# Performance work log

Measured on AMD Instinct MI355X. Metric: run time of the kernel, lower is better.

Reference implementation:

```python
import jax, jax.numpy as jnp
import numpy as np

H, W, DIM, B, K = 28, 28, 384, 64, 1
EPS = 1e-5


def setup_inputs() -> dict:
    key = jax.random.key(0)
    k1, k2, k3 = jax.random.split(key, 3)
    L = 1 + K * H * W
    x = jax.random.normal(k1, (B, L, DIM), dtype=jnp.float32)
    w_reduction = jax.random.normal(k2, (2 * DIM, 4 * DIM), dtype=jnp.float32) * 0.02
    w_convert = jax.random.normal(k3, (2 * DIM, DIM), dtype=jnp.float32) * 0.02
    ln_gamma = jnp.ones((4 * DIM,), dtype=jnp.float32)
    ln_beta = jnp.zeros((4 * DIM,), dtype=jnp.float32)
    return {"x": x, "w_reduction": w_reduction, "w_convert": w_convert,
            "ln_gamma": ln_gamma, "ln_beta": ln_beta}


def reference(x, w_reduction, w_convert, ln_gamma, ln_beta):
    Bb, L, C = x.shape
    k = (L - 1) // (H * W)
    cls_token = x[:, 0:1, :]                      # [B,1,C]
    feat = x[:, 1:, :].reshape(Bb, k, H, W, C)
    x0 = feat[:, :, 0::2, 0::2, :]                # [B,k,H/2,W/2,C]
    x1 = feat[:, :, 1::2, 0::2, :]
    x2 = feat[:, :, 0::2, 1::2, :]
    x3 = feat[:, :, 1::2, 1::2, :]
    m = jnp.concatenate([x0, x1, x2, x3], axis=-1)  # [B,k,H/2,W/2,4C]
    m = m.reshape(Bb, k, -1, 4 * C)
    # LayerNorm over last dim
    mu = jnp.mean(m, axis=-1, keepdims=True)
    var = jnp.mean(jnp.square(m - mu), axis=-1, keepdims=True)
    m = (m - mu) * jax.lax.rsqrt(var + EPS) * ln_gamma + ln_beta
    red = jnp.einsum('bknf,of->bkno', m, w_reduction).reshape(Bb, -1, 2 * C)
    cls_out = jnp.einsum('bic,oc->bio', cls_token, w_convert)  # [B,1,2C]
    return jnp.concatenate([cls_out, red], axis=1)
```

## Files before the change

### kernel.cpp

```cpp
#include <hip/hip_runtime.h>
#include <hip/hip_bf16.h>

#define DIMC 384
#define LL 785
#define FDIM 1536
#define ODIM 768
#define NPATCH 196
#define MROWS 12544
#define BATCH 64

typedef __attribute__((ext_vector_type(8))) short bf16x8;
typedef __attribute__((ext_vector_type(4))) float floatx4;
typedef __attribute__((ext_vector_type(4))) unsigned short ushort4v;

#define WS_WBF_OFF  38535168
#define WS_BIAS_OFF 40894464

__device__ __forceinline__ unsigned short f2bf(float f) {
  union { float f; unsigned int u; } v; v.f = f;
  unsigned int u = v.u + 0x7fffu + ((v.u >> 16) & 1u);
  return (unsigned short)(u >> 16);
}

__device__ __forceinline__ void gload_lds16(const void* g, void* l) {
  __builtin_amdgcn_global_load_lds(
      (const __attribute__((address_space(1))) unsigned int*)g,
      (__attribute__((address_space(3))) unsigned int*)l, 16, 0, 0);
}

__global__ __launch_bounds__(256) void prep_kernel(
    const float* __restrict__ x, const float* __restrict__ wred,
    const float* __restrict__ wconv, const float* __restrict__ gamma,
    const float* __restrict__ beta, unsigned short* __restrict__ anorm,
    unsigned short* __restrict__ wbf, float* __restrict__ bias,
    float* __restrict__ out) {
  const int blk = blockIdx.x;
  const int t = threadIdx.x;
  const int wv = t >> 6;
  const int lane = t & 63;

  if (blk < 3136) {
    int gw = blk * 4 + wv;
    int b = gw / NPATCH;
    int n = gw - b * NPATCH;
    int i = n / 14;
    int j = n - i * 14;
    const float* xb = x + ((size_t)b * LL + 1) * DIMC;
    float4 v[6];
    float s = 0.f, s2 = 0.f;
#pragma unroll
    for (int c = 0; c < 6; ++c) {
      int f = lane * 4 + c * 256;
      int q = f / 384;
      int cc = f - q * 384;
      int off = ((i * 2 + (q & 1)) * 28 + (j * 2 + ((q >> 1) & 1))) * DIMC + cc;
      v[c] = *reinterpret_cast<const float4*>(xb + off);
      s  += v[c].x + v[c].y + v[c].z + v[c].w;
      s2 += v[c].x * v[c].x + v[c].y * v[c].y + v[c].z * v[c].z + v[c].w * v[c].w;
    }
#pragma unroll
    for (int o = 1; o < 64; o <<= 1) {
      s  += __shfl_xor(s, o);
      s2 += __shfl_xor(s2, o);
    }
    float mu = s * (1.f / FDIM);
    float var = s2 * (1.f / FDIM) - mu * mu;
    float rs = rsqrtf(var + 1e-5f);
    float nmu = -mu * rs;
    unsigned short* arow = anorm + (size_t)gw * FDIM;
#pragma unroll
    for (int c = 0; c < 6; ++c) {
      int f = lane * 4 + c * 256;
      union { ushort4v u4; __hip_bfloat162 h[2]; } u;
      u.h[0] = __float22bfloat162_rn(
          make_float2(v[c].x * rs + nmu, v[c].y * rs + nmu));
      u.h[1] = __float22bfloat162_rn(
          make_float2(v[c].z * rs + nmu, v[c].w * rs + nmu));
      *reinterpret_cast<ushort4v*>(arow + f) = u.u4;
    }
  } else if (blk < 4288) {
    int idx4 = (blk - 3136) * 256 + t;
    int e0 = idx4 * 4;
    int f = e0 % FDIM;
    float4 w = *reinterpret_cast<const float4*>(wred + e0);
    float4 g = *reinterpret_cast<const float4*>(gamma + f);
    ushort4v u;
    u.x = f2bf(w.x * g.x); u.y = f2bf(w.y * g.y);
    u.z = f2bf(w.z * g.z); u.w = f2bf(w.w * g.w);
    *reinterpret_cast<ushort4v*>(wbf + e0) = u;
  } else if (blk < 4480) {
    int o = (blk - 4288) * 4 + wv;
    const float* wr = wred + (size_t)o * FDIM;
    float s = 0.f;
#pragma unroll
    for (int c = 0; c < 6; ++c) {
      int f = lane * 4 + c * 256;
      float4 w = *reinterpret_cast<const float4*>(wr + f);
      float4 be = *reinterpret_cast<const float4*>(beta + f);
      s += w.x * be.x + w.y * be.y + w.z * be.z + w.w * be.w;
    }
#pragma unroll
    for (int o2 = 32; o2 > 0; o2 >>= 1) s += __shfl_down(s, o2);
    if (lane == 0) bias[o] = s;
  } else {
    __shared__ float xs[DIMC];
    int idx = blk - 4480;
    int b = idx / 3;
    int ch = idx - b * 3;
    for (int c = t; c < DIMC; c += 256) xs[c] = x[(size_t)b * LL * DIMC + c];
    __syncthreads();
    int o = ch * 256 + t;
    const float* wr = wconv + (size_t)o * DIMC;
    float acc = 0.f;
#pragma unroll 4
    for (int c = 0; c < DIMC; c += 4) {
      float4 w = *reinterpret_cast<const float4*>(wr + c);
      acc += w.x * xs[c] + w.y * xs[c + 1] + w.z * xs[c + 2] + w.w * xs[c + 3];
    }
    out[(size_t)b * 197 * ODIM + o] = acc;
  }
}

__global__ __launch_bounds__(256) void gemm_kernel(
    const unsigned short* __restrict__ anorm,
    const unsigned short* __restrict__ wbf,
    const float* __restrict__ bias, float* __restrict__ out) {
  __shared__ unsigned short As[128 * 64];
  __shared__ unsigned short Bs[128 * 64];

  const int t = threadIdx.x;
  const int mBase = blockIdx.y * 128;
  const int nBase = blockIdx.x * 128;

  const unsigned short* agp[4];
  const unsigned short* bgp[4];
  unsigned int ldsoff[4];
#pragma unroll
  for (int p = 0; p < 4; ++p) {
    int s = p * 256 + t;
    int r = s >> 3;
    int cs = (s & 7) ^ (r & 7);
    agp[p] = anorm + (size_t)(mBase + r) * FDIM + cs * 8;
    bgp[p] = wbf + (size_t)(nBase + r) * FDIM + cs * 8;
    ldsoff[p] = (unsigned)s * 8;
  }

  const int wv = t >> 6;
  const int lane = t & 63;
  const int ln15 = lane & 15;
  const int quad = lane >> 4;
  const int wm = wv >> 1;
  const int wn = wv & 1;

  unsigned int aoff[4][2], boff[4][2];
#pragma unroll
  for (int mt = 0; mt < 4; ++mt) {
#pragma unroll
    for (int h = 0; h < 2; ++h) {
      int rA = wm * 64 + mt * 16 + ln15;
      aoff[mt][h] = (unsigned)(rA * 64 + (((h * 4 + quad) ^ (rA & 7)) * 8));
      int rB = wn * 64 + mt * 16 + ln15;
      boff[mt][h] = (unsigned)(rB * 64 + (((h * 4 + quad) ^ (rB & 7)) * 8));
    }
  }

  floatx4 acc[4][4];
#pragma unroll
  for (int mt = 0; mt < 4; ++mt)
#pragma unroll
    for (int nt = 0; nt < 4; ++nt)
      acc[mt][nt] = floatx4{0.f, 0.f, 0.f, 0.f};

  for (int kt = 0; kt < FDIM / 64; ++kt) {
    if (kt) __syncthreads();
#pragma unroll
    for (int p = 0; p < 4; ++p) {
      gload_lds16(agp[p], &As[ldsoff[p]]);
      gload_lds16(bgp[p], &Bs[ldsoff[p]]);
      agp[p] += 64;
      bgp[p] += 64;
    }
    __syncthreads();

#pragma unroll
    for (int h = 0; h < 2; ++h) {
      bf16x8 af[4], bfr[4];
#pragma unroll
      for (int mt = 0; mt < 4; ++mt)
        af[mt] = *reinterpret_cast<const bf16x8*>(&As[aoff[mt][h]]);
#pragma unroll
      for (int nt = 0; nt < 4; ++nt)
        bfr[nt] = *reinterpret_cast<const bf16x8*>(&Bs[boff[nt][h]]);
#pragma unroll
      for (int mt = 0; mt < 4; ++mt)
#pragma unroll
        for (int nt = 0; nt < 4; ++nt)
          acc[mt][nt] = __builtin_amdgcn_mfma_f32_16x16x32_bf16(
              af[mt], bfr[nt], acc[mt][nt], 0, 0, 0);
    }
  }

  float bs[4];
#pragma unroll
  for (int nt = 0; nt < 4; ++nt)
    bs[nt] = bias[nBase + wn * 64 + nt * 16 + ln15];
#pragma unroll
  for (int mt = 0; mt < 4; ++mt) {
#pragma unroll
    for (int r = 0; r < 4; ++r) {
      int m = mBase + wm * 64 + mt * 16 + quad * 4 + r;
      int b = m / NPATCH;
      int n = m - b * NPATCH;
      float* orow = out + ((size_t)b * 197 + 1 + n) * ODIM + nBase + wn * 64;
#pragma unroll
      for (int nt = 0; nt < 4; ++nt)
        orow[nt * 16 + ln15] = acc[mt][nt][r] + bs[nt];
    }
  }
}

extern "C" void kernel_launch(void* const* d_in, const int* in_sizes, int n_in,
                              void* d_out, int out_size, void* d_ws, size_t ws_size,
                              hipStream_t stream) {
  const float* x     = (const float*)d_in[0];
  const float* wred  = (const float*)d_in[1];
  const float* wconv = (const float*)d_in[2];
  const float* gamma = (const float*)d_in[3];
  const float* beta  = (const float*)d_in[4];
  float* out = (float*)d_out;

  unsigned short* anorm = (unsigned short*)d_ws;
  unsigned short* wbf   = (unsigned short*)((char*)d_ws + WS_WBF_OFF);
  float* bias           = (float*)((char*)d_ws + WS_BIAS_OFF);

  prep_kernel<<<dim3(4672), 256, 0, stream>>>(x, wred, wconv, gamma, beta,
                                              anorm, wbf, bias, out);
  gemm_kernel<<<dim3(ODIM / 128, MROWS / 128), 256, 0, stream>>>(anorm, wbf,
                                                                 bias, out);
}
```

Before: 205.4 us.

## Rework prep blocks for multi-row norm and remap GEMM tiles per XCD

The prep kernel now has each wave process four LayerNorm rows, taking statistics in a first pass and then re-reading x for the normalize/store pass instead of holding values in registers. Block ranges are reordered so the cls GEMV and bias blocks come first, and the cls GEMV is vectorized with two accumulators. The GEMM uses a 1D grid with an XCD-aware tile remap so neighbouring tiles share the same L2, and stores the output with nontemporal stores. These changes target prep occupancy and launch count, L2 locality for the GEMM, and cache pollution from output writes, at the cost of a second read of x that relies on cache hits.

New measurement: 185.1 us. 9.9% less time.

```diff
diff --git a/kernel.cpp b/kernel.cpp
--- a/kernel.cpp
+++ b/kernel.cpp
@@ -15,6 +15,12 @@
 
 #define WS_WBF_OFF  38535168
 #define WS_BIAS_OFF 40894464
+
+#define PB_CLS   0
+#define PB_NORM  192
+#define PB_BIAS  976
+#define PB_WBF   1168
+#define PREP_BLOCKS 2320
 
 __device__ __forceinline__ unsigned short f2bf(float f) {
   union { float f; unsigned int u; } v; v.f = f;
@@ -39,47 +45,102 @@
   const int wv = t >> 6;
   const int lane = t & 63;
 
-  if (blk < 3136) {
-    int gw = blk * 4 + wv;
-    int b = gw / NPATCH;
-    int n = gw - b * NPATCH;
-    int i = n / 14;
-    int j = n - i * 14;
-    const float* xb = x + ((size_t)b * LL + 1) * DIMC;
-    float4 v[6];
-    float s = 0.f, s2 = 0.f;
+  if (blk >= PB_NORM && blk < PB_BIAS) {
+    int radd[6];
 #pragma unroll
     for (int c = 0; c < 6; ++c) {
       int f = lane * 4 + c * 256;
       int q = f / 384;
       int cc = f - q * 384;
-      int off = ((i * 2 + (q & 1)) * 28 + (j * 2 + ((q >> 1) & 1))) * DIMC + cc;
-      v[c] = *reinterpret_cast<const float4*>(xb + off);
-      s  += v[c].x + v[c].y + v[c].z + v[c].w;
-      s2 += v[c].x * v[c].x + v[c].y * v[c].y + v[c].z * v[c].z + v[c].w * v[c].w;
+      radd[c] = ((q & 1) * 28 + ((q >> 1) & 1)) * DIMC + cc;
+    }
+    const int wvid = (blk - PB_NORM) * 4 + wv;
+    const int g0 = wvid * 4;
+
+    size_t bo[4];
+    float s[4], s2[4];
+#pragma unroll
+    for (int r = 0; r < 4; ++r) {
+      int gw = g0 + r;
+      int b = gw / NPATCH;
+      int n = gw - b * NPATCH;
+      int i = n / 14;
+      int j = n - i * 14;
+      bo[r] = (size_t)b * LL * DIMC + DIMC + (size_t)((i * 56 + j * 2) * DIMC);
+      s[r] = 0.f; s2[r] = 0.f;
+#pragma unroll
+      for (int c = 0; c < 6; ++c) {
+        float4 v = *reinterpret_cast<const float4*>(x + bo[r] + radd[c]);
+        s[r]  += v.x + v.y + v.z + v.w;
+        s2[r] += v.x * v.x + v.y * v.y + v.z * v.z + v.w * v.w;
+      }
     }
 #pragma unroll
     for (int o = 1; o < 64; o <<= 1) {
-      s  += __shfl_xor(s, o);
-      s2 += __shfl_xor(s2, o);
-    }
-    float mu = s * (1.f / FDIM);
-    float var = s2 * (1.f / FDIM) - mu * mu;
-    float rs = rsqrtf(var + 1e-5f);
-    float nmu = -mu * rs;
-    unsigned short* arow = anorm + (size_t)gw * FDIM;
+#pragma unroll
+      for (int r = 0; r < 4; ++r) {
+        s[r]  += __shfl_xor(s[r], o);
+        s2[r] += __shfl_xor(s2[r], o);
+      }
+    }
+    const float* xr;
+    { unsigned long long u = (unsigned long long)x;
+      asm volatile("" : "+s"(u));
+      xr = (const float*)u; }
+#pragma unroll
+    for (int r = 0; r < 4; ++r) {
+      float mu = s[r] * (1.f / FDIM);
+      float var = s2[r] * (1.f / FDIM) - mu * mu;
+      float rs = rsqrtf(var + 1e-5f);
+      float nmu = -mu * rs;
+      unsigned short* arow = anorm + (size_t)(g0 + r) * FDIM;
+#pragma unroll
+      for (int c = 0; c < 6; ++c) {
+        float4 v = *reinterpret_cast<const float4*>(xr + bo[r] + radd[c]);
+        union { ushort4v u4; __hip_bfloat162 h[2]; } u;
+        u.h[0] = __float22bfloat162_rn(
+            make_float2(v.x * rs + nmu, v.y * rs + nmu));
+        u.h[1] = __float22bfloat162_rn(
+            make_float2(v.z * rs + nmu, v.w * rs + nmu));
+        *reinterpret_cast<ushort4v*>(arow + lane * 4 + c * 256) = u.u4;
+      }
+    }
+  } else if (blk < PB_NORM) {
+    __shared__ float xs[DIMC];
+    int idx = blk;
+    int b = idx / 3;
+    int ch = idx - b * 3;
+    for (int c = t; c < DIMC; c += 256) xs[c] = x[(size_t)b * LL * DIMC + c];
+    __syncthreads();
+    int o = ch * 256 + t;
+    const float* wr = wconv + (size_t)o * DIMC;
+    float a0 = 0.f, a1 = 0.f;
+#pragma unroll 4
+    for (int c = 0; c < DIMC; c += 8) {
+      float4 w0 = *reinterpret_cast<const float4*>(wr + c);
+      float4 w1 = *reinterpret_cast<const float4*>(wr + c + 4);
+      float4 p0 = *reinterpret_cast<const float4*>(&xs[c]);
+      float4 p1 = *reinterpret_cast<const float4*>(&xs[c + 4]);
+      a0 += w0.x * p0.x + w0.y * p0.y + w0.z * p0.z + w0.w * p0.w;
+      a1 += w1.x * p1.x + w1.y * p1.y + w1.z * p1.z + w1.w * p1.w;
+    }
+    out[(size_t)b * 197 * ODIM + o] = a0 + a1;
+  } else if (blk < PB_WBF) {
+    int o = (blk - PB_BIAS) * 4 + wv;
+    const float* wr = wred + (size_t)o * FDIM;
+    float s = 0.f;
 #pragma unroll
     for (int c = 0; c < 6; ++c) {
       int f = lane * 4 + c * 256;
-      union { ushort4v u4; __hip_bfloat162 h[2]; } u;
-      u.h[0] = __float22bfloat162_rn(
-          make_float2(v[c].x * rs + nmu, v[c].y * rs + nmu));
-      u.h[1] = __float22bfloat162_rn(
-          make_float2(v[c].z * rs + nmu, v[c].w * rs + nmu));
-      *reinterpret_cast<ushort4v*>(arow + f) = u.u4;
-    }
-  } else if (blk < 4288) {
-    int idx4 = (blk - 3136) * 256 + t;
+      float4 w = *reinterpret_cast<const float4*>(wr + f);
+      float4 be = *reinterpret_cast<const float4*>(beta + f);
+      s += w.x * be.x + w.y * be.y + w.z * be.z + w.w * be.w;
+    }
+#pragma unroll
+    for (int o2 = 32; o2 > 0; o2 >>= 1) s += __shfl_down(s, o2);
+    if (lane == 0) bias[o] = s;
+  } else {
+    int idx4 = (blk - PB_WBF) * 256 + t;
     int e0 = idx4 * 4;
     int f = e0 % FDIM;
     float4 w = *reinterpret_cast<const float4*>(wred + e0);
@@ -88,36 +149,6 @@
     u.x = f2bf(w.x * g.x); u.y = f2bf(w.y * g.y);
     u.z = f2bf(w.z * g.z); u.w = f2bf(w.w * g.w);
     *reinterpret_cast<ushort4v*>(wbf + e0) = u;
-  } else if (blk < 4480) {
-    int o = (blk - 4288) * 4 + wv;
-    const float* wr = wred + (size_t)o * FDIM;
-    float s = 0.f;
-#pragma unroll
-    for (int c = 0; c < 6; ++c) {
-      int f = lane * 4 + c * 256;
-      float4 w = *reinterpret_cast<const float4*>(wr + f);
-      float4 be = *reinterpret_cast<const float4*>(beta + f);
-      s += w.x * be.x + w.y * be.y + w.z * be.z + w.w * be.w;
-    }
-#pragma unroll
-    for (int o2 = 32; o2 > 0; o2 >>= 1) s += __shfl_down(s, o2);
-    if (lane == 0) bias[o] = s;
-  } else {
-    __shared__ float xs[DIMC];
-    int idx = blk - 4480;
-    int b = idx / 3;
-    int ch = idx - b * 3;
-    for (int c = t; c < DIMC; c += 256) xs[c] = x[(size_t)b * LL * DIMC + c];
-    __syncthreads();
-    int o = ch * 256 + t;
-    const float* wr = wconv + (size_t)o * DIMC;
-    float acc = 0.f;
-#pragma unroll 4
-    for (int c = 0; c < DIMC; c += 4) {
-      float4 w = *reinterpret_cast<const float4*>(wr + c);
-      acc += w.x * xs[c] + w.y * xs[c + 1] + w.z * xs[c + 2] + w.w * xs[c + 3];
-    }
-    out[(size_t)b * 197 * ODIM + o] = acc;
   }
 }
 
@@ -129,8 +160,17 @@
   __shared__ unsigned short Bs[128 * 64];
 
   const int t = threadIdx.x;
-  const int mBase = blockIdx.y * 128;
-  const int nBase = blockIdx.x * 128;
+
+  const int NWG = (ODIM / 128) * (MROWS / 128);
+  const int qq = NWG >> 3, rr = NWG & 7;
+  int bid = blockIdx.x;
+  int xcd = bid & 7, pos = bid >> 3;
+  int wg = (xcd < rr) ? xcd * (qq + 1) + pos
+                      : rr * (qq + 1) + (xcd - rr) * qq + pos;
+  int my = wg / 6;
+  int nx = wg - my * 6;
+  const int mBase = my * 128;
+  const int nBase = nx * 128;
 
   const unsigned short* agp[4];
   const unsigned short* bgp[4];
@@ -214,7 +254,8 @@
       float* orow = out + ((size_t)b * 197 + 1 + n) * ODIM + nBase + wn * 64;
 #pragma unroll
       for (int nt = 0; nt < 4; ++nt)
-        orow[nt * 16 + ln15] = acc[mt][nt][r] + bs[nt];
+        __builtin_nontemporal_store(acc[mt][nt][r] + bs[nt],
+                                    &orow[nt * 16 + ln15]);
     }
   }
 }
@@ -233,8 +274,9 @@
   unsigned short* wbf   = (unsigned short*)((char*)d_ws + WS_WBF_OFF);
   float* bias           = (float*)((char*)d_ws + WS_BIAS_OFF);
 
-  prep_kernel<<<dim3(4672), 256, 0, stream>>>(x, wred, wconv, gamma, beta,
-                                              anorm, wbf, bias, out);
-  gemm_kernel<<<dim3(ODIM / 128, MROWS / 128), 256, 0, stream>>>(anorm, wbf,
-                                                                 bias, out);
-}
+  prep_kernel<<<dim3(PREP_BLOCKS), 256, 0, stream>>>(x, wred, wconv, gamma,
+                                                     beta, anorm, wbf, bias,
+                                                     out);
+  gemm_kernel<<<dim3((ODIM / 128) * (MROWS / 128)), 256, 0, stream>>>(
+      anorm, wbf, bias, out);
+}
```
